# Performance work log

Hardware: AMD Instinct MI355X
Metric: run time of the kernel (lower is better)

The kernel has to match this reference:

```python
import jax, jax.numpy as jnp
import numpy as np

N_NODES = 100000  # total nodes (60k type-a + 40k type-b)
N_EDGES = 3200000


def spmm(rows, cols, vals, x):
    # y[r] = sum_e vals[e] * x[cols[e]] for edges with rows[e] == r  (COO SpMM)
    return jax.ops.segment_sum(vals[:, None] * x[cols], rows, num_segments=N_NODES)


def setup_inputs() -> dict:
    key = jax.random.key(0)
    ks = jax.random.split(key, 12)
    d_a, d_b, n_hid, n_out = 256, 128, 256, 64
    s = lambda d: (1.0 / np.sqrt(d)).astype(np.float32)
    return {
        "x_a": jax.random.normal(ks[0], (60000, d_a), dtype=jnp.float32),
        "x_b": jax.random.normal(ks[1], (40000, d_b), dtype=jnp.float32),
        "rows": jax.random.randint(ks[2], (N_EDGES,), 0, N_NODES, dtype=jnp.int32),
        "cols": jax.random.randint(ks[3], (N_EDGES,), 0, N_NODES, dtype=jnp.int32),
        "vals": jax.random.uniform(ks[4], (N_EDGES,), dtype=jnp.float32),
        "W1a": jax.random.normal(ks[5], (d_a, n_hid), dtype=jnp.float32) * s(d_a),
        "b1a": jnp.zeros((n_hid,), dtype=jnp.float32),
        "W1b": jax.random.normal(ks[6], (d_b, n_hid), dtype=jnp.float32) * s(d_b),
        "b1b": jnp.zeros((n_hid,), dtype=jnp.float32),
        "Wf": jax.random.normal(ks[7], (n_hid, n_hid), dtype=jnp.float32) * s(n_hid),
        "bf": jnp.zeros((n_hid,), dtype=jnp.float32),
        "W2": jax.random.normal(ks[8], (n_hid, n_out), dtype=jnp.float32) * s(n_hid),
        "b2": jnp.zeros((n_out,), dtype=jnp.float32),
    }


def reference(x_a, x_b, rows, cols, vals, W1a, b1a, W1b, b1b, Wf, bf, W2, b2):
    # per-type Linear + ReLU (dropout p=0 -> identity in eval/reference)
    h_a = jax.nn.relu(x_a @ W1a + b1a)  # [60000, n_hid]
    h_b = jax.nn.relu(x_b @ W1b + b1b)  # [40000, n_hid]
    x = jnp.concatenate([h_a, h_b], axis=0)  # [N_NODES, n_hid]
    # hop - 1 = 1 intermediate hop: Linear -> SpMM -> ReLU
    x = x @ Wf + bf
    x = spmm(rows, cols, vals, x)
    x = jax.nn.relu(x)
    # output projection then final SpMM aggregation
    x = x @ W2 + b2
    x = spmm(rows, cols, vals, x)  # [N_NODES, n_out]
    return x
```

## Files before the change

kernel.cpp:

```cpp
#include <hip/hip_runtime.h>

#define NN 100000
#define NE 3200000
#define NA 60000
#define NB 40000
#define NHID 256
#define NOUT 64

#define RPB 64
#define NBUCK 1563
#define PBLK 256
#define CHUNK 12500

#define WT_BLKS 704
#define G1_BLKS 469
#define G2_BLKS 313
#define G3_BLKS 782

typedef unsigned short u16;
typedef unsigned int u32;
typedef __attribute__((ext_vector_type(8))) short short8;
typedef __attribute__((ext_vector_type(4))) float f32x4;

__device__ __forceinline__ float bf2f(u16 u) {
  return __uint_as_float(((u32)u) << 16);
}
__device__ __forceinline__ u16 f2bf(float f) {
  u32 u = __float_as_uint(f);
  u32 r = (u + 0x7fffu + ((u >> 16) & 1u)) >> 16;
  return (u16)r;
}
__device__ __forceinline__ float i8f(u32 dw, int b) {
  return (float)((int)(dw << (24 - 8 * b)) >> 24);
}
__device__ __forceinline__ u16 f2h(float f) {
  _Float16 h = (_Float16)f;
  u16 r;
  __builtin_memcpy(&r, &h, 2);
  return r;
}
__device__ __forceinline__ float h2f(u32 b15) {
  u16 hb = (u16)b15;
  _Float16 h;
  __builtin_memcpy(&h, &hb, 2);
  return (float)h;
}

__device__ __forceinline__ void gload_lds16(const void* gsrc, void* ldst) {
  __builtin_amdgcn_global_load_lds(
      (const __attribute__((address_space(1))) void*)gsrc,
      (__attribute__((address_space(3))) void*)ldst, 16, 0, 0);
}

template <int QUANT>
__device__ __forceinline__ void gemm8_body(
    int bx, const u16* __restrict__ A, const u16* __restrict__ Bt,
    const float* __restrict__ bias, void* __restrict__ Cout,
    float* __restrict__ scales, int M, int K, u16* As, u16* Bs) {
  const int tid = threadIdx.x;
  const int w = tid >> 6;
  const int lane = tid & 63;
  const int bm = bx * 128;
  const int wr = w >> 2;
  const int wc = w & 3;

  f32x4 acc[4][4];
#pragma unroll
  for (int i = 0; i < 4; ++i)
#pragma unroll
    for (int j = 0; j < 4; ++j) acc[i][j] = (f32x4)0.f;

  for (int k0 = 0; k0 < K; k0 += 32) {
    {
      const int row = w * 16 + (lane >> 2);
      int rg = bm + row;
      if (rg > M - 1) rg = M - 1;
      const int c = (lane & 3) ^ ((row >> 1) & 3);
      gload_lds16(A + (size_t)rg * K + k0 + c * 8, &As[w * 512]);
    }
#pragma unroll
    for (int s = 0; s < 2; ++s) {
      const int inst = w * 2 + s;
      const int row = inst * 16 + (lane >> 2);
      const int c = (lane & 3) ^ ((row >> 1) & 3);
      gload_lds16(Bt + (size_t)row * K + k0 + c * 8, &Bs[inst * 512]);
    }
    __syncthreads();

    const int kc = lane >> 4;
    short8 af[4], bfr[4];
#pragma unroll
    for (int i = 0; i < 4; ++i) {
      const int row = wr * 64 + i * 16 + (lane & 15);
      const int ch = kc ^ ((row >> 1) & 3);
      af[i] = *reinterpret_cast<const short8*>(&As[row * 32 + ch * 8]);
    }
#pragma unroll
    for (int j = 0; j < 4; ++j) {
      const int row = wc * 64 + j * 16 + (lane & 15);
      const int ch = kc ^ ((row >> 1) & 3);
      bfr[j] = *reinterpret_cast<const short8*>(&Bs[row * 32 + ch * 8]);
    }
#pragma unroll
    for (int i = 0; i < 4; ++i)
#pragma unroll
      for (int j = 0; j < 4; ++j)
        acc[i][j] = __builtin_amdgcn_mfma_f32_16x16x32_bf16(af[i], bfr[j],
                                                            acc[i][j], 0, 0, 0);
    __syncthreads();
  }

  if constexpr (QUANT == 1) {
    float bv[4];
#pragma unroll
    for (int j = 0; j < 4; ++j) bv[j] = bias[wc * 64 + j * 16 + (lane & 15)];
    const int g = wc;
    u32* zq = (u32*)Cout;
#pragma unroll
    for (int i = 0; i < 4; ++i) {
#pragma unroll
      for (int r = 0; r < 4; ++r) {
        float o[4];
#pragma unroll
        for (int j = 0; j < 4; ++j) o[j] = acc[i][j][r] + bv[j];
        float am = fmaxf(fmaxf(fabsf(o[0]), fabsf(o[1])),
                         fmaxf(fabsf(o[2]), fabsf(o[3])));
#pragma unroll
        for (int mk = 1; mk < 16; mk <<= 1) am = fmaxf(am, __shfl_xor(am, mk));
        const float sinv = am > 0.f ? 127.f / am : 0.f;
        const float scv = am > 0.f ? am / 127.f : 0.f;
        const int q0 = __float2int_rn(o[0] * sinv);
        const int q1 = __float2int_rn(o[1] * sinv);
        const int q2 = __float2int_rn(o[2] * sinv);
        const int q3 = __float2int_rn(o[3] * sinv);
        const u32 dw = (q0 & 0xff) | ((q1 & 0xff) << 8) | ((q2 & 0xff) << 16) |
                       ((q3 & 0xff) << 24);
        const int row = bm + wr * 64 + i * 16 + (lane >> 4) * 4 + r;
        if (row < M) {
          zq[(size_t)row * 64 + g * 16 + (lane & 15)] = dw;
          if ((lane & 15) == 0) scales[(size_t)row * 4 + g] = scv;
        }
      }
    }
  } else {
    u16* C = (u16*)Cout;
#pragma unroll
    for (int i = 0; i < 4; ++i) {
#pragma unroll
      for (int j = 0; j < 4; ++j) {
        const int col = wc * 64 + j * 16 + (lane & 15);
        const float bv = bias[col];
#pragma unroll
        for (int r = 0; r < 4; ++r) {
          const int row = bm + wr * 64 + i * 16 + (lane >> 4) * 4 + r;
          if (row < M) {
            float o = fmaxf(acc[i][j][r] + bv, 0.f);
            C[(size_t)row * 256 + col] = f2bf(o);
          }
        }
      }
    }
  }
}

__device__ __forceinline__ void gemm8_af32(
    int bx, const float* __restrict__ Af, const u16* __restrict__ Bt,
    const float* __restrict__ bias, u16* __restrict__ C, int M, int K,
    u16* As, u16* Bs) {
  const int tid = threadIdx.x;
  const int w = tid >> 6;
  const int lane = tid & 63;
  const int bm = bx * 128;
  const int wr = w >> 2;
  const int wc = w & 3;

  f32x4 acc[4][4];
#pragma unroll
  for (int i = 0; i < 4; ++i)
#pragma unroll
    for (int j = 0; j < 4; ++j) acc[i][j] = (f32x4)0.f;

  const int arow = tid >> 2;
  const int aq = tid & 3;
  int arg = bm + arow;
  if (arg > M - 1) arg = M - 1;
  const int asw = (arow >> 1) & 3;

  for (int k0 = 0; k0 < K; k0 += 32) {
#pragma unroll
    for (int s = 0; s < 2; ++s) {
      const int inst = w * 2 + s;
      const int row = inst * 16 + (lane >> 2);
      const int c = (lane & 3) ^ ((row >> 1) & 3);
      gload_lds16(Bt + (size_t)row * K + k0 + c * 8, &Bs[inst * 512]);
    }
    {
      const float4* src =
          reinterpret_cast<const float4*>(Af + (size_t)arg * K + k0 + aq * 8);
      const float4 v0 = src[0], v1 = src[1];
      short8 ch;
      ch[0] = (short)f2bf(v0.x); ch[1] = (short)f2bf(v0.y);
      ch[2] = (short)f2bf(v0.z); ch[3] = (short)f2bf(v0.w);
      ch[4] = (short)f2bf(v1.x); ch[5] = (short)f2bf(v1.y);
      ch[6] = (short)f2bf(v1.z); ch[7] = (short)f2bf(v1.w);
      reinterpret_cast<short8*>(As + arow * 32)[aq ^ asw] = ch;
    }
    __syncthreads();

    const int kc = lane >> 4;
    short8 af[4], bfr[4];
#pragma unroll
    for (int i = 0; i < 4; ++i) {
      const int row = wr * 64 + i * 16 + (lane & 15);
      const int ch = kc ^ ((row >> 1) & 3);
      af[i] = *reinterpret_cast<const short8*>(&As[row * 32 + ch * 8]);
    }
#pragma unroll
    for (int j = 0; j < 4; ++j) {
      const int row = wc * 64 + j * 16 + (lane & 15);
      const int ch = kc ^ ((row >> 1) & 3);
      bfr[j] = *reinterpret_cast<const short8*>(&Bs[row * 32 + ch * 8]);
    }
#pragma unroll
    for (int i = 0; i < 4; ++i)
#pragma unroll
      for (int j = 0; j < 4; ++j)
        acc[i][j] = __builtin_amdgcn_mfma_f32_16x16x32_bf16(af[i], bfr[j],
                                                            acc[i][j], 0, 0, 0);
    __syncthreads();
  }

#pragma unroll
  for (int i = 0; i < 4; ++i) {
#pragma unroll
    for (int j = 0; j < 4; ++j) {
      const int col = wc * 64 + j * 16 + (lane & 15);
      const float bv = bias[col];
#pragma unroll
      for (int r = 0; r < 4; ++r) {
        const int row = bm + wr * 64 + i * 16 + (lane >> 4) * 4 + r;
        if (row < M) {
          float o = fmaxf(acc[i][j][r] + bv, 0.f);
          C[(size_t)row * 256 + col] = f2bf(o);
        }
      }
    }
  }
}

__global__ __launch_bounds__(256) void gemm4_q8(
    const u16* __restrict__ A, const u16* __restrict__ Bt,
    const float* __restrict__ bias, u32* __restrict__ zq,
    float* __restrict__ scales, int M, int K) {
  __shared__ __align__(16) u16 As[128 * 32];
  __shared__ __align__(16) u16 Bs[64 * 32];
  const int tid = threadIdx.x;
  const int w = tid >> 6;
  const int lane = tid & 63;
  const int bm = blockIdx.x * 128;

  f32x4 acc[2][4];
#pragma unroll
  for (int i = 0; i < 2; ++i)
#pragma unroll
    for (int j = 0; j < 4; ++j) acc[i][j] = (f32x4)0.f;

  for (int k0 = 0; k0 < K; k0 += 32) {
#pragma unroll
    for (int s = 0; s < 2; ++s) {
      const int inst = w * 2 + s;
      const int row = inst * 16 + (lane >> 2);
      int rg = bm + row;
      if (rg > M - 1) rg = M - 1;
      const int c = (lane & 3) ^ ((row >> 1) & 3);
      gload_lds16(A + (size_t)rg * K + k0 + c * 8, &As[inst * 512]);
    }
    {
      const int row = w * 16 + (lane >> 2);
      const int c = (lane & 3) ^ ((row >> 1) & 3);
      gload_lds16(Bt + (size_t)row * K + k0 + c * 8, &Bs[w * 512]);
    }
    __syncthreads();

    const int kc = lane >> 4;
    short8 af[2], bfr[4];
#pragma unroll
    for (int i = 0; i < 2; ++i) {
      const int row = w * 32 + i * 16 + (lane & 15);
      const int ch = kc ^ ((row >> 1) & 3);
      af[i] = *reinterpret_cast<const short8*>(&As[row * 32 + ch * 8]);
    }
#pragma unroll
    for (int j = 0; j < 4; ++j) {
      const int row = j * 16 + (lane & 15);
      const int ch = kc ^ ((row >> 1) & 3);
      bfr[j] = *reinterpret_cast<const short8*>(&Bs[row * 32 + ch * 8]);
    }
#pragma unroll
    for (int i = 0; i < 2; ++i)
#pragma unroll
      for (int j = 0; j < 4; ++j)
        acc[i][j] = __builtin_amdgcn_mfma_f32_16x16x32_bf16(af[i], bfr[j],
                                                            acc[i][j], 0, 0, 0);
    __syncthreads();
  }

  float bv[4];
#pragma unroll
  for (int j = 0; j < 4; ++j) bv[j] = bias[j * 16 + (lane & 15)];
#pragma unroll
  for (int i = 0; i < 2; ++i) {
#pragma unroll
    for (int r = 0; r < 4; ++r) {
      float o[4];
#pragma unroll
      for (int j = 0; j < 4; ++j) o[j] = acc[i][j][r] + bv[j];
      float am = fmaxf(fmaxf(fabsf(o[0]), fabsf(o[1])),
                       fmaxf(fabsf(o[2]), fabsf(o[3])));
#pragma unroll
      for (int mk = 1; mk < 16; mk <<= 1) am = fmaxf(am, __shfl_xor(am, mk));
      const float sinv = am > 0.f ? 127.f / am : 0.f;
      const float scv = am > 0.f ? am / 127.f : 0.f;
      const int q0 = __float2int_rn(o[0] * sinv);
      const int q1 = __float2int_rn(o[1] * sinv);
      const int q2 = __float2int_rn(o[2] * sinv);
      const int q3 = __float2int_rn(o[3] * sinv);
      const u32 dw = (q0 & 0xff) | ((q1 & 0xff) << 8) | ((q2 & 0xff) << 16) |
                     ((q3 & 0xff) << 24);
      const int row = bm + w * 32 + i * 16 + (lane >> 4) * 4 + r;
      if (row < M) {
        zq[(size_t)row * 16 + (lane & 15)] = dw;
        if ((lane & 15) == 0) scales[row] = scv;
      }
    }
  }
}

__global__ __launch_bounds__(256) void prep(
    const float* __restrict__ W1a, const float* __restrict__ W1b,
    const float* __restrict__ Wf, const float* __restrict__ W2,
    u16* __restrict__ W1at, u16* __restrict__ W1bt, u16* __restrict__ Wft,
    u16* __restrict__ W2t, const int* __restrict__ rows,
    int* __restrict__ cnt) {
  __shared__ int hsh[NBUCK];
  const int b = blockIdx.x;
  const int tid = threadIdx.x;
  if (b < WT_BLKS) {
    const int i = b * 256 + tid;
    if (i < 65536) {
      const int n = i >> 8, k = i & 255;
      W1at[i] = f2bf(W1a[k * 256 + n]);
    } else if (i < 98304) {
      const int t = i - 65536;
      const int n = t >> 7, k = t & 127;
      W1bt[t] = f2bf(W1b[k * 256 + n]);
    } else if (i < 163840) {
      const int t = i - 98304;
      const int n = t >> 8, k = t & 255;
      Wft[t] = f2bf(Wf[k * 256 + n]);
    } else if (i < 180224) {
      const int t = i - 163840;
      const int n = t >> 8, p = t & 255;
      const int f = ((p >> 6) << 6) + ((p & 3) << 4) + ((p >> 2) & 15);
      W2t[t] = f2bf(W2[f * 64 + n]);
    }
  } else {
    const int blk = b - WT_BLKS;
    for (int i = tid; i < NBUCK; i += 256) hsh[i] = 0;
    __syncthreads();
    const int s = blk * CHUNK;
    const int e = s + CHUNK;
    for (int i = s + tid; i < e; i += 256) atomicAdd(&hsh[rows[i] >> 6], 1);
    __syncthreads();
    for (int i = tid; i < NBUCK; i += 256) cnt[i * PBLK + blk] = hsh[i];
  }
}

__global__ __launch_bounds__(512) void gemm12_s1(
    const float* __restrict__ xa, const u16* __restrict__ W1at,
    const float* __restrict__ b1a, const float* __restrict__ xb,
    const u16* __restrict__ W1bt, const float* __restrict__ b1b,
    u16* __restrict__ h, int* __restrict__ cnt, int* __restrict__ btot) {
  __shared__ __align__(16) u16 As[128 * 32];
  __shared__ __align__(16) u16 Bs[256 * 32];
  const int b = blockIdx.x;
  if (b < G1_BLKS) {
    gemm8_af32(b, xa, W1at, b1a, h, NA, 256, As, Bs);
  } else if (b < G1_BLKS + G2_BLKS) {
    gemm8_af32(b - G1_BLKS, xb, W1bt, b1b, h + (size_t)NA * NHID, NB, 128, As,
               Bs);
  } else {
    int* lds = (int*)As;
    const int bu = b - (G1_BLKS + G2_BLKS);
    const int t = threadIdx.x;
    const int v = (t < PBLK) ? cnt[bu * PBLK + t] : 0;
    lds[t] = v;
    __syncthreads();
#pragma unroll
    for (int off = 1; off < PBLK; off <<= 1) {
      const int x = (t >= off) ? lds[t - off] : 0;
      __syncthreads();
      lds[t] += x;
      __syncthreads();
    }
    if (t < PBLK) cnt[bu * PBLK + t] = lds[t] - v;
    if (t == PBLK - 1) btot[bu] = lds[t];
  }
}

__global__ __launch_bounds__(512) void gemm3_s2_p3(
    const u16* __restrict__ h, const u16* __restrict__ Wft,
    const float* __restrict__ bfv, u32* __restrict__ zq,
    float* __restrict__ zscale, const int* __restrict__ btot,
    int* __restrict__ bstart, const int* __restrict__ rows,
    const int* __restrict__ cols, const float* __restrict__ vals,
    const int* __restrict__ cnt, int2* __restrict__ edges) {
  __shared__ __align__(16) u16 As[128 * 32];
  __shared__ __align__(16) u16 Bs[256 * 32];
  const int b = blockIdx.x;
  const int t = threadIdx.x;
  if (b < G3_BLKS) {
    gemm8_body<1>(b, h, Wft, bfv, zq, zscale, NN, 256, As, Bs);
  } else if (b == G3_BLKS) {
    int* lds = (int*)As;
    int carry = 0;
    for (int base = 0; base < NBUCK; base += 512) {
      const int i = base + t;
      const int v = (i < NBUCK) ? btot[i] : 0;
      lds[t] = v;
      __syncthreads();
#pragma unroll
      for (int off = 1; off < 512; off <<= 1) {
        const int x = (t >= off) ? lds[t - off] : 0;
        __syncthreads();
        lds[t] += x;
        __syncthreads();
      }
      const int excl = lds[t] - v;
      const int tot = lds[511];
      if (i < NBUCK) bstart[i] = carry + excl;
      __syncthreads();
      carry += tot;
    }
    if (t == 0) bstart[NBUCK] = NE;
  } else {
    const int blk = b - (G3_BLKS + 1);
    int* lbs = (int*)As;
    int* tmp = (int*)Bs;
    int carry = 0;
    for (int base = 0; base < NBUCK; base += 512) {
      const int i = base + t;
      const int v = (i < NBUCK) ? btot[i] : 0;
      tmp[t] = v;
      __syncthreads();
#pragma unroll
      for (int off = 1; off < 512; off <<= 1) {
        const int x = (t >= off) ? tmp[t - off] : 0;
        __syncthreads();
        tmp[t] += x;
        __syncthreads();
      }
      if (i < NBUCK) lbs[i] = carry + tmp[t] - v;
      const int tot = tmp[511];
      __syncthreads();
      carry += tot;
    }
    for (int bu = t; bu < NBUCK; bu += 512) lbs[bu] += cnt[bu * PBLK + blk];
    __syncthreads();
    const int s = blk * CHUNK;
    const int e = s + CHUNK;
    for (int i = s + t; i < e; i += 512) {
      const int r = rows[i];
      const int pos = atomicAdd(&lbs[r >> 6], 1);
      edges[pos] =
          make_int2(cols[i] | ((r & 63) << 17), __float_as_int(vals[i]));
    }
  }
}

__global__ __launch_bounds__(256) void sort_bucket(
    const int* __restrict__ bstart, const int2* __restrict__ edges,
    u32* __restrict__ edges2, int* __restrict__ rptr) {
  __shared__ int hist[RPB];
  __shared__ int sc[RPB];
  __shared__ int cur[RPB];
  const int bu = blockIdx.x;
  const int t = threadIdx.x;
  const int s = bstart[bu], e = bstart[bu + 1];
  if (t < RPB) hist[t] = 0;
  __syncthreads();
  for (int i = s + t; i < e; i += 256)
    atomicAdd(&hist[(edges[i].x >> 17) & 63], 1);
  __syncthreads();
  const int hv = (t < RPB) ? hist[t] : 0;
  if (t < RPB) sc[t] = hv;
  __syncthreads();
#pragma unroll
  for (int off = 1; off < RPB; off <<= 1) {
    const int x = (t >= off && t < RPB) ? sc[t - off] : 0;
    __syncthreads();
    if (t < RPB) sc[t] += x;
    __syncthreads();
  }
  if (t < RPB) {
    const int base = s + sc[t] - hv;
    cur[t] = base;
    const int grow = bu * RPB + t;
    if (grow < NN) rptr[grow] = base;
  }
  if (bu == 0 && t == 0) rptr[NN] = NE;
  __syncthreads();
  for (int i = s + t; i < e; i += 256) {
    const int2 ed = edges[i];
    const int lr = (ed.x >> 17) & 63;
    const int pos = atomicAdd(&cur[lr], 1);
    edges2[pos] = (u32)(ed.x & 0x1FFFF) |
                  ((u32)f2h(__int_as_float(ed.y)) << 17);
  }
}

__global__ __launch_bounds__(256) void spmm256_q8(
    const int* __restrict__ ptr, const u32* __restrict__ edges,
    const u32* __restrict__ Zq, const float* __restrict__ scales,
    u16* __restrict__ Yb) {
  const int wid = (int)((blockIdx.x * (size_t)256 + threadIdx.x) >> 6);
  const int lane = threadIdx.x & 63;
  if (wid >= NN) return;
  const int s = ptr[wid], e = ptr[wid + 1];
  const int gsel = lane >> 4;
  float a0 = 0.f, a1 = 0.f, a2 = 0.f, a3 = 0.f;
  int j = s;
  for (; j + 7 < e; j += 8) {
    u32 ed[8];
#pragma unroll
    for (int q = 0; q < 8; ++q) ed[q] = edges[j + q];
    u32 dw[8];
    float sc[8];
#pragma unroll
    for (int q = 0; q < 8; ++q) {
      const int c = ed[q] & 0x1FFFF;
      dw[q] = Zq[(size_t)c * 64 + lane];
      sc[q] = scales[(size_t)c * 4 + gsel];
    }
#pragma unroll
    for (int q = 0; q < 8; ++q) {
      const float vs = h2f(ed[q] >> 17) * sc[q];
      a0 += vs * i8f(dw[q], 0);
      a1 += vs * i8f(dw[q], 1);
      a2 += vs * i8f(dw[q], 2);
      a3 += vs * i8f(dw[q], 3);
    }
  }
  for (; j < e; ++j) {
    const u32 ed = edges[j];
    const int c = ed & 0x1FFFF;
    const u32 dw = Zq[(size_t)c * 64 + lane];
    const float vs = h2f(ed >> 17) * scales[(size_t)c * 4 + gsel];
    a0 += vs * i8f(dw, 0);
    a1 += vs * i8f(dw, 1);
    a2 += vs * i8f(dw, 2);
    a3 += vs * i8f(dw, 3);
  }
  ushort4 o;
  o.x = f2bf(fmaxf(a0, 0.f));
  o.y = f2bf(fmaxf(a1, 0.f));
  o.z = f2bf(fmaxf(a2, 0.f));
  o.w = f2bf(fmaxf(a3, 0.f));
  reinterpret_cast<ushort4*>(Yb + (size_t)wid * 256)[lane] = o;
}

__global__ __launch_bounds__(256) void spmm64_q8(
    const int* __restrict__ ptr, const u32* __restrict__ edges,
    const u32* __restrict__ Z2q, const float* __restrict__ zsc2,
    float* __restrict__ Y) {
  const int wid = (int)((blockIdx.x * (size_t)256 + threadIdx.x) >> 6);
  const int lane = threadIdx.x & 63;
  if (wid >= NN) return;
  const int s = ptr[wid], e = ptr[wid + 1];
  const int dwi = lane & 15;
  const int byi = lane >> 4;
  float acc = 0.f;
  int j = s;
  for (; j + 7 < e; j += 8) {
    u32 ed[8];
#pragma unroll
    for (int q = 0; q < 8; ++q) ed[q] = edges[j + q];
    u32 dw[8];
    float sc[8];
#pragma unroll
    for (int q = 0; q < 8; ++q) {
      const int c = ed[q] & 0x1FFFF;
      dw[q] = Z2q[(size_t)c * 16 + dwi];
      sc[q] = zsc2[c];
    }
#pragma unroll
    for (int q = 0; q < 8; ++q)
      acc += h2f(ed[q] >> 17) * sc[q] * i8f(dw[q], byi);
  }
  for (; j < e; ++j) {
    const u32 ed = edges[j];
    const int c = ed & 0x1FFFF;
    acc += h2f(ed >> 17) * zsc2[c] * i8f(Z2q[(size_t)c * 16 + dwi], byi);
  }
  Y[(size_t)wid * 64 + lane] = acc;
}

extern "C" void kernel_launch(void* const* d_in, const int* in_sizes, int n_in,
                              void* d_out, int out_size, void* d_ws,
                              size_t ws_size, hipStream_t stream) {
  const float* x_a  = (const float*)d_in[0];
  const float* x_b  = (const float*)d_in[1];
  const int*   rows = (const int*)d_in[2];
  const int*   cols = (const int*)d_in[3];
  const float* vals = (const float*)d_in[4];
  const float* W1a  = (const float*)d_in[5];
  const float* b1a  = (const float*)d_in[6];
  const float* W1b  = (const float*)d_in[7];
  const float* b1b  = (const float*)d_in[8];
  const float* Wf   = (const float*)d_in[9];
  const float* bf   = (const float*)d_in[10];
  const float* W2   = (const float*)d_in[11];
  const float* b2   = (const float*)d_in[12];
  float* out = (float*)d_out;

  char* p = (char*)d_ws;
  u16* h    = (u16*)p;  p += (size_t)NN * NHID * 2;
  u32* zq   = (u32*)p;  p += (size_t)NN * 64 * 4;
  float* zscale = (float*)p; p += (size_t)NN * 4 * 4;
  u32* z2q  = (u32*)p;  p += (size_t)NN * 16 * 4;
  float* zsc2 = (float*)p; p += (size_t)NN * 4;
  u32* edges2 = (u32*)p;  p += (size_t)NE * 4;
  u16* W1at = (u16*)p;  p += 256 * 256 * 2;
  u16* W1bt = (u16*)p;  p += 256 * 128 * 2;
  u16* Wft  = (u16*)p;  p += 256 * 256 * 2;
  u16* W2t  = (u16*)p;  p += 64 * 256 * 2;
  int2* edges = (int2*)p; p += (size_t)NE * 8;
  int* cnt    = (int*)p;  p += (size_t)NBUCK * PBLK * 4;
  int* btot   = (int*)p;  p += (size_t)((NBUCK + 3) & ~3) * 4;
  int* bstart = (int*)p;  p += (size_t)((NBUCK + 4) & ~3) * 4;
  int* rptr   = (int*)p;  p += (size_t)(NN + 4) * 4;
  u16* s1b = h;

  prep<<<WT_BLKS + PBLK, 256, 0, stream>>>(W1a, W1b, Wf, W2, W1at, W1bt, Wft,
                                           W2t, rows, cnt);

  gemm12_s1<<<G1_BLKS + G2_BLKS + NBUCK, 512, 0, stream>>>(
      x_a, W1at, b1a, x_b, W1bt, b1b, h, cnt, btot);

  gemm3_s2_p3<<<G3_BLKS + 1 + PBLK, 512, 0, stream>>>(
      h, Wft, bf, zq, zscale, btot, bstart, rows, cols, vals, cnt, edges);

  sort_bucket<<<NBUCK, 256, 0, stream>>>(bstart, edges, edges2, rptr);

  spmm256_q8<<<(NN * 64 + 255) / 256, 256, 0, stream>>>(rptr, edges2, zq,
                                                        zscale, s1b);
  gemm4_q8<<<G3_BLKS, 256, 0, stream>>>(s1b, W2t, b2, z2q, zsc2, NN, 256);
  spmm64_q8<<<(NN * 64 + 255) / 256, 256, 0, stream>>>(rptr, edges2, z2q,
                                                       zsc2, out);
}
```

Baseline: 423.0 us.

## Split Wf GEMM across scatter and sort launches; use offset-uint8 dequant in SpMMs

The Wf GEMM is split in half. The first half runs alongside the bucket scatter and the second half is fused into the per-bucket sort kernel, so GEMM blocks overlap with the sorting work and one launch's worth of serialisation goes away. The int8 quantisation now stores values offset by 128 as unsigned bytes. The SpMM kernels unpack them with cheap mask/shift-to-float conversions and subtract 128 times the running sum of weights at the end, replacing the sign-extending extraction. The sort kernel now runs 512 threads per block, which may leave many threads idle on small buckets, and the offset correction can add some cancellation error.

```diff
diff --git a/kernel.cpp b/kernel.cpp
--- a/kernel.cpp
+++ b/kernel.cpp
@@ -16,6 +16,8 @@
 #define G1_BLKS 469
 #define G2_BLKS 313
 #define G3_BLKS 782
+#define G3A 391
+#define G3B 391
 
 typedef unsigned short u16;
 typedef unsigned int u32;
@@ -29,9 +31,6 @@
   u32 u = __float_as_uint(f);
   u32 r = (u + 0x7fffu + ((u >> 16) & 1u)) >> 16;
   return (u16)r;
-}
-__device__ __forceinline__ float i8f(u32 dw, int b) {
-  return (float)((int)(dw << (24 - 8 * b)) >> 24);
 }
 __device__ __forceinline__ u16 f2h(float f) {
   _Float16 h = (_Float16)f;
@@ -129,10 +128,10 @@
         for (int mk = 1; mk < 16; mk <<= 1) am = fmaxf(am, __shfl_xor(am, mk));
         const float sinv = am > 0.f ? 127.f / am : 0.f;
         const float scv = am > 0.f ? am / 127.f : 0.f;
-        const int q0 = __float2int_rn(o[0] * sinv);
-        const int q1 = __float2int_rn(o[1] * sinv);
-        const int q2 = __float2int_rn(o[2] * sinv);
-        const int q3 = __float2int_rn(o[3] * sinv);
+        const int q0 = __float2int_rn(o[0] * sinv) + 128;
+        const int q1 = __float2int_rn(o[1] * sinv) + 128;
+        const int q2 = __float2int_rn(o[2] * sinv) + 128;
+        const int q3 = __float2int_rn(o[3] * sinv) + 128;
         const u32 dw = (q0 & 0xff) | ((q1 & 0xff) << 8) | ((q2 & 0xff) << 16) |
                        ((q3 & 0xff) << 24);
         const int row = bm + wr * 64 + i * 16 + (lane >> 4) * 4 + r;
@@ -321,10 +320,10 @@
       for (int mk = 1; mk < 16; mk <<= 1) am = fmaxf(am, __shfl_xor(am, mk));
       const float sinv = am > 0.f ? 127.f / am : 0.f;
       const float scv = am > 0.f ? am / 127.f : 0.f;
-      const int q0 = __float2int_rn(o[0] * sinv);
-      const int q1 = __float2int_rn(o[1] * sinv);
-      const int q2 = __float2int_rn(o[2] * sinv);
-      const int q3 = __float2int_rn(o[3] * sinv);
+      const int q0 = __float2int_rn(o[0] * sinv) + 128;
+      const int q1 = __float2int_rn(o[1] * sinv) + 128;
+      const int q2 = __float2int_rn(o[2] * sinv) + 128;
+      const int q3 = __float2int_rn(o[3] * sinv) + 128;
       const u32 dw = (q0 & 0xff) | ((q1 & 0xff) << 8) | ((q2 & 0xff) << 16) |
                      ((q3 & 0xff) << 24);
       const int row = bm + w * 32 + i * 16 + (lane >> 4) * 4 + r;
@@ -408,7 +407,7 @@
   }
 }
 
-__global__ __launch_bounds__(512) void gemm3_s2_p3(
+__global__ __launch_bounds__(512) void gemm3a_s2_p3(
     const u16* __restrict__ h, const u16* __restrict__ Wft,
     const float* __restrict__ bfv, u32* __restrict__ zq,
     float* __restrict__ zscale, const int* __restrict__ btot,
@@ -419,9 +418,9 @@
   __shared__ __align__(16) u16 Bs[256 * 32];
   const int b = blockIdx.x;
   const int t = threadIdx.x;
-  if (b < G3_BLKS) {
+  if (b < G3A) {
     gemm8_body<1>(b, h, Wft, bfv, zq, zscale, NN, 256, As, Bs);
-  } else if (b == G3_BLKS) {
+  } else if (b == G3A) {
     int* lds = (int*)As;
     int carry = 0;
     for (int base = 0; base < NBUCK; base += 512) {
@@ -444,7 +443,7 @@
     }
     if (t == 0) bstart[NBUCK] = NE;
   } else {
-    const int blk = b - (G3_BLKS + 1);
+    const int blk = b - (G3A + 1);
     int* lbs = (int*)As;
     int* tmp = (int*)Bs;
     int carry = 0;
@@ -478,44 +477,54 @@
   }
 }
 
-__global__ __launch_bounds__(256) void sort_bucket(
-    const int* __restrict__ bstart, const int2* __restrict__ edges,
-    u32* __restrict__ edges2, int* __restrict__ rptr) {
+__global__ __launch_bounds__(512) void gemm3b_sort(
+    const u16* __restrict__ h, const u16* __restrict__ Wft,
+    const float* __restrict__ bfv, u32* __restrict__ zq,
+    float* __restrict__ zscale, const int* __restrict__ bstart,
+    const int2* __restrict__ edges, u32* __restrict__ edges2,
+    int* __restrict__ rptr) {
+  __shared__ __align__(16) u16 As[128 * 32];
+  __shared__ __align__(16) u16 Bs[256 * 32];
   __shared__ int hist[RPB];
   __shared__ int sc[RPB];
   __shared__ int cur[RPB];
-  const int bu = blockIdx.x;
+  const int b = blockIdx.x;
   const int t = threadIdx.x;
-  const int s = bstart[bu], e = bstart[bu + 1];
-  if (t < RPB) hist[t] = 0;
-  __syncthreads();
-  for (int i = s + t; i < e; i += 256)
-    atomicAdd(&hist[(edges[i].x >> 17) & 63], 1);
-  __syncthreads();
-  const int hv = (t < RPB) ? hist[t] : 0;
-  if (t < RPB) sc[t] = hv;
-  __syncthreads();
-#pragma unroll
-  for (int off = 1; off < RPB; off <<= 1) {
-    const int x = (t >= off && t < RPB) ? sc[t - off] : 0;
-    __syncthreads();
-    if (t < RPB) sc[t] += x;
-    __syncthreads();
-  }
-  if (t < RPB) {
-    const int base = s + sc[t] - hv;
-    cur[t] = base;
-    const int grow = bu * RPB + t;
-    if (grow < NN) rptr[grow] = base;
-  }
-  if (bu == 0 && t == 0) rptr[NN] = NE;
-  __syncthreads();
-  for (int i = s + t; i < e; i += 256) {
-    const int2 ed = edges[i];
-    const int lr = (ed.x >> 17) & 63;
-    const int pos = atomicAdd(&cur[lr], 1);
-    edges2[pos] = (u32)(ed.x & 0x1FFFF) |
-                  ((u32)f2h(__int_as_float(ed.y)) << 17);
+  if (b < G3B) {
+    gemm8_body<1>(b + G3A, h, Wft, bfv, zq, zscale, NN, 256, As, Bs);
+  } else {
+    const int bu = b - G3B;
+    const int s = bstart[bu], e = bstart[bu + 1];
+    if (t < RPB) hist[t] = 0;
+    __syncthreads();
+    for (int i = s + t; i < e; i += 512)
+      atomicAdd(&hist[(edges[i].x >> 17) & 63], 1);
+    __syncthreads();
+    const int hv = (t < RPB) ? hist[t] : 0;
+    if (t < RPB) sc[t] = hv;
+    __syncthreads();
+#pragma unroll
+    for (int off = 1; off < RPB; off <<= 1) {
+      const int x = (t >= off && t < RPB) ? sc[t - off] : 0;
+      __syncthreads();
+      if (t < RPB) sc[t] += x;
+      __syncthreads();
+    }
+    if (t < RPB) {
+      const int base = s + sc[t] - hv;
+      cur[t] = base;
+      const int grow = bu * RPB + t;
+      if (grow < NN) rptr[grow] = base;
+    }
+    if (bu == 0 && t == 0) rptr[NN] = NE;
+    __syncthreads();
+    for (int i = s + t; i < e; i += 512) {
+      const int2 ed = edges[i];
+      const int lr = (ed.x >> 17) & 63;
+      const int pos = atomicAdd(&cur[lr], 1);
+      edges2[pos] = (u32)(ed.x & 0x1FFFF) |
+                    ((u32)f2h(__int_as_float(ed.y)) << 17);
+    }
   }
 }
 
@@ -528,7 +537,7 @@
   if (wid >= NN) return;
   const int s = ptr[wid], e = ptr[wid + 1];
   const int gsel = lane >> 4;
-  float a0 = 0.f, a1 = 0.f, a2 = 0.f, a3 = 0.f;
+  float a0 = 0.f, a1 = 0.f, a2 = 0.f, a3 = 0.f, S = 0.f;
   int j = s;
   for (; j + 7 < e; j += 8) {
     u32 ed[8];
@@ -545,10 +554,11 @@
 #pragma unroll
     for (int q = 0; q < 8; ++q) {
       const float vs = h2f(ed[q] >> 17) * sc[q];
-      a0 += vs * i8f(dw[q], 0);
-      a1 += vs * i8f(dw[q], 1);
-      a2 += vs * i8f(dw[q], 2);
-      a3 += vs * i8f(dw[q], 3);
+      S += vs;
+      a0 += vs * (float)(dw[q] & 0xffu);
+      a1 += vs * (float)((dw[q] >> 8) & 0xffu);
+      a2 += vs * (float)((dw[q] >> 16) & 0xffu);
+      a3 += vs * (float)(dw[q] >> 24);
     }
   }
   for (; j < e; ++j) {
@@ -556,16 +566,18 @@
     const int c = ed & 0x1FFFF;
     const u32 dw = Zq[(size_t)c * 64 + lane];
     const float vs = h2f(ed >> 17) * scales[(size_t)c * 4 + gsel];
-    a0 += vs * i8f(dw, 0);
-    a1 += vs * i8f(dw, 1);
-    a2 += vs * i8f(dw, 2);
-    a3 += vs * i8f(dw, 3);
-  }
+    S += vs;
+    a0 += vs * (float)(dw & 0xffu);
+    a1 += vs * (float)((dw >> 8) & 0xffu);
+    a2 += vs * (float)((dw >> 16) & 0xffu);
+    a3 += vs * (float)(dw >> 24);
+  }
+  const float corr = 128.f * S;
   ushort4 o;
-  o.x = f2bf(fmaxf(a0, 0.f));
-  o.y = f2bf(fmaxf(a1, 0.f));
-  o.z = f2bf(fmaxf(a2, 0.f));
-  o.w = f2bf(fmaxf(a3, 0.f));
+  o.x = f2bf(fmaxf(a0 - corr, 0.f));
+  o.y = f2bf(fmaxf(a1 - corr, 0.f));
+  o.z = f2bf(fmaxf(a2 - corr, 0.f));
+  o.w = f2bf(fmaxf(a3 - corr, 0.f));
   reinterpret_cast<ushort4*>(Yb + (size_t)wid * 256)[lane] = o;
 }
 
@@ -578,8 +590,8 @@
   if (wid >= NN) return;
   const int s = ptr[wid], e = ptr[wid + 1];
   const int dwi = lane & 15;
-  const int byi = lane >> 4;
-  float acc = 0.f;
+  const int bsh = (lane >> 4) * 8;
+  float acc = 0.f, S = 0.f;
   int j = s;
   for (; j + 7 < e; j += 8) {
     u32 ed[8];
@@ -594,15 +606,20 @@
       sc[q] = zsc2[c];
     }
 #pragma unroll
-    for (int q = 0; q < 8; ++q)
-      acc += h2f(ed[q] >> 17) * sc[q] * i8f(dw[q], byi);
+    for (int q = 0; q < 8; ++q) {
+      const float vs = h2f(ed[q] >> 17) * sc[q];
+      S += vs;
+      acc += vs * (float)((dw[q] >> bsh) & 0xffu);
+    }
   }
   for (; j < e; ++j) {
     const u32 ed = edges[j];
     const int c = ed & 0x1FFFF;
-    acc += h2f(ed >> 17) * zsc2[c] * i8f(Z2q[(size_t)c * 16 + dwi], byi);
-  }
-  Y[(size_t)wid * 64 + lane] = acc;
+    const float vs = h2f(ed >> 17) * zsc2[c];
+    S += vs;
+    acc += vs * (float)((Z2q[(size_t)c * 16 + dwi] >> bsh) & 0xffu);
+  }
+  Y[(size_t)wid * 64 + lane] = acc - 128.f * S;
 }
 
 extern "C" void kernel_launch(void* const* d_in, const int* in_sizes, int n_in,
@@ -647,10 +664,11 @@
   gemm12_s1<<<G1_BLKS + G2_BLKS + NBUCK, 512, 0, stream>>>(
       x_a, W1at, b1a, x_b, W1bt, b1b, h, cnt, btot);
 
-  gemm3_s2_p3<<<G3_BLKS + 1 + PBLK, 512, 0, stream>>>(
+  gemm3a_s2_p3<<<G3A + 1 + PBLK, 512, 0, stream>>>(
       h, Wft, bf, zq, zscale, btot, bstart, rows, cols, vals, cnt, edges);
 
-  sort_bucket<<<NBUCK, 256, 0, stream>>>(bstart, edges, edges2, rptr);
+  gemm3b_sort<<<G3B + NBUCK, 512, 0, stream>>>(h, Wft, bf, zq, zscale, bstart,
+                                               edges, edges2, rptr);
 
   spmm256_q8<<<(NN * 64 + 255) / 256, 256, 0, stream>>>(rptr, edges2, zq,
                                                         zscale, s1b);
```

Measured after the change: 424.0 us. About the same (+0.2%).
